# Kernel optimization log

Hardware: AMD Instinct MI355X
Metric: run time of the kernel (lower is better)

Reference implementation:

```python
import jax, jax.numpy as jnp
import numpy as np

B, N, DIM = 4, 2048, 3
H = 128          # hidden
K = 32           # num_neighbours
L = 4            # num_layers
OUT = 6          # out_per_particle


def _dense_init(key, fan_in, fan_out):
    kw, kb = jax.random.split(key)
    w = jax.random.normal(kw, (fan_in, fan_out), jnp.float32) / np.sqrt(fan_in)
    b = jnp.zeros((fan_out,), jnp.float32)
    return w, b


def setup_inputs() -> dict:
    key = jax.random.key(0)
    ks = jax.random.split(key, 8)
    x = jax.random.normal(ks[0], (B, N, DIM), jnp.float32)
    embed_w, embed_b = _dense_init(ks[1], DIM, H)
    # per-layer stacked params
    miw, mib, mow, mob, uiw, uib, uow, uob = [], [], [], [], [], [], [], []
    for l in range(L):
        k0, k1, k2, k3 = jax.random.split(jax.random.fold_in(ks[2], l), 4)
        w, b = _dense_init(k0, 2 * H + 1, H); miw.append(w); mib.append(b)
        w, b = _dense_init(k1, H, H);         mow.append(w); mob.append(b)
        w, b = _dense_init(k2, 2 * H, H);     uiw.append(w); uib.append(b)
        w, b = _dense_init(k3, H, H);         uow.append(w); uob.append(b)
    out_w, out_b = _dense_init(ks[3], H, OUT)
    return {
        'x': x,
        'embed_w': embed_w, 'embed_b': embed_b,
        'msg_in_w': jnp.stack(miw), 'msg_in_b': jnp.stack(mib),
        'msg_out_w': jnp.stack(mow), 'msg_out_b': jnp.stack(mob),
        'upd_in_w': jnp.stack(uiw), 'upd_in_b': jnp.stack(uib),
        'upd_out_w': jnp.stack(uow), 'upd_out_b': jnp.stack(uob),
        'out_w': out_w, 'out_b': out_b,
    }


def reference(x, embed_w, embed_b,
              msg_in_w, msg_in_b, msg_out_w, msg_out_b,
              upd_in_w, upd_in_b, upd_out_w, upd_out_b,
              out_w, out_b):
    act = jax.nn.silu
    n = x.shape[-2]
    # per-particle embed: (B,N,H)
    h = x @ embed_w + embed_b
    # pairwise squared distances (B,N,N), plain Euclidean (geometry=None)
    diff = x[..., :, None, :] - x[..., None, :, :]
    d_sq = jnp.sum(diff * diff, axis=-1)
    eye = jnp.eye(n, dtype=bool)
    d_sq = jnp.where(eye, jnp.inf, d_sq)
    neg_topk, idx_topk = jax.lax.top_k(-d_sq, K)      # (B,N,K)
    d_nearest = jnp.sqrt(jnp.maximum(-neg_topk, 0.0))  # (B,N,K)

    gather = jax.vmap(lambda hb, ib: hb[ib])  # (N,H),(N,K)->(N,K,H) over batch
    n_layers = msg_in_w.shape[0]
    for l in range(n_layers):
        nb = gather(h, idx_topk)                               # (B,N,K,H)
        node_i = jnp.broadcast_to(h[..., :, None, :], nb.shape)
        msg_inp = jnp.concatenate([node_i, nb, d_nearest[..., None]], axis=-1)
        msg = act(msg_inp @ msg_in_w[l] + msg_in_b[l]) @ msg_out_w[l] + msg_out_b[l]
        agg = jnp.sum(msg, axis=-2)                            # (B,N,H)
        upd_inp = jnp.concatenate([h, agg], axis=-1)
        upd = act(upd_inp @ upd_in_w[l] + upd_in_b[l]) @ upd_out_w[l] + upd_out_b[l]
        h = h + upd
    return h @ out_w + out_b
```

## Files before the change

kernel.cpp:

```cpp
#include <hip/hip_runtime.h>
#include <math.h>

#define B_ 4
#define N_ 2048
#define H_ 128
#define K_ 32
#define L_ 4
#define OUT_ 6
#define BN_ (B_*N_)
#define NPB_L 16
#define LBLK 512

typedef __attribute__((ext_vector_type(8))) short short8;
typedef __attribute__((ext_vector_type(4))) float f32x4;

#define LDW (H_ + 8)
#define LAYER_W 98304
#define OFF_W1A 0
#define OFF_W1C 16384
#define OFF_W2  32768
#define OFF_U1  49152
#define OFF_U2  81920
#define SCAP 256
#define KNN_ROWS 4
#define KNN_BLKS (BN_/KNN_ROWS)
#define PREP_BLKS (L_*LAYER_W/256)

#define LOG2E 1.44269504088896340736f
#define LN2   0.69314718055994530942f

__device__ __forceinline__ float silu_f(float x) {
    return __fdividef(x, 1.0f + __expf(-x));
}
__device__ __forceinline__ float silu_y(float y) {
    return __fdividef(y, 1.0f + __builtin_amdgcn_exp2f(-y));
}
__device__ __forceinline__ short f2b(float f) {
    unsigned u = __float_as_uint(f);
    return (short)((u + 0x7FFFu + ((u >> 16) & 1u)) >> 16);
}
__device__ __forceinline__ float b2f(short s) {
    return __uint_as_float(((unsigned)(unsigned short)s) << 16);
}
__device__ __forceinline__ unsigned pack2(short lo, short hi) {
    return (unsigned)(unsigned short)lo | ((unsigned)(unsigned short)hi << 16);
}
__device__ __forceinline__ int mbcnt64(unsigned long long m) {
    return __builtin_amdgcn_mbcnt_hi((unsigned)(m >> 32),
           __builtin_amdgcn_mbcnt_lo((unsigned)m, 0));
}

__global__ __launch_bounds__(256) void k_front(
    const float* __restrict__ x, int* __restrict__ nidx, float* __restrict__ ndist,
    const float* __restrict__ miw, const float* __restrict__ mow,
    const float* __restrict__ uiw, const float* __restrict__ uow,
    short* __restrict__ wt,
    const float* __restrict__ ew, const float* __restrict__ eb,
    const float* __restrict__ mib, float* __restrict__ Epack)
{
    __shared__ float xsx[N_], xsy[N_], xsz[N_];
    __shared__ unsigned skey[KNN_ROWS][SCAP];
    __shared__ int      sid [KNN_ROWS][SCAP];

    if (blockIdx.x >= KNN_BLKS + PREP_BLKS) {
        int t = threadIdx.x;
        int which = t >> 7, n = t & 127;
        const float* W = miw + (size_t)(which ? 128 : 0) * H_;
        float E0 = 0.f, E1 = 0.f, E2 = 0.f, Eb = 0.f;
        for (int k = 0; k < 128; ++k) {
            float w = W[(size_t)k*H_ + n];
            E0 = fmaf(ew[k],       w, E0);
            E1 = fmaf(ew[128 + k], w, E1);
            E2 = fmaf(ew[256 + k], w, E2);
            Eb = fmaf(eb[k],       w, Eb);
        }
        float* dst = Epack + which * 512;
        dst[0*128 + n] = E0 * LOG2E;
        dst[1*128 + n] = E1 * LOG2E;
        dst[2*128 + n] = E2 * LOG2E;
        dst[3*128 + n] = (Eb + (which ? 0.f : mib[n])) * LOG2E;
        return;
    }
    if (blockIdx.x >= KNN_BLKS) {
        int gid = (blockIdx.x - KNN_BLKS) * 256 + threadIdx.x;
        int l = gid / LAYER_W, o = gid - l * LAYER_W;
        float v;
        if (o < OFF_W1C) {
            int n = o >> 7, k = o & 127;
            v = miw[(size_t)l*257*H_ + k*H_ + n] * LOG2E;
        } else if (o < OFF_W2) {
            int oo = o - OFF_W1C, n = oo >> 7, k = oo & 127;
            v = miw[(size_t)l*257*H_ + (128 + k)*H_ + n] * LOG2E;
        } else if (o < OFF_U1) {
            int oo = o - OFF_W2, n = oo >> 7, k = oo & 127;
            v = mow[(size_t)l*H_*H_ + k*H_ + n];
        } else if (o < OFF_U2) {
            int oo = o - OFF_U1, n = oo >> 8, k = oo & 255;
            v = uiw[(size_t)l*2*H_*H_ + k*H_ + n];
        } else {
            int oo = o - OFF_U2, n = oo >> 7, k = oo & 127;
            v = uow[(size_t)l*H_*H_ + k*H_ + n];
        }
        wt[gid] = f2b(v);
        return;
    }

    int b  = blockIdx.x / (N_/KNN_ROWS);
    int i0 = (blockIdx.x % (N_/KNN_ROWS)) * KNN_ROWS;
    const float* xb = x + (size_t)b*N_*3;
    for (int t = threadIdx.x; t < N_*3; t += 256) {
        float v = xb[t];
        int q = t / 3, r = t - q*3;
        float* dst = (r == 0) ? xsx : (r == 1) ? xsy : xsz;
        dst[q] = v;
    }
    __syncthreads();

    int wave = threadIdx.x >> 6, lane = threadIdx.x & 63;
    int i = i0 + wave;
    float xix = xsx[i], xiy = xsy[i], xiz = xsz[i];

    unsigned u[N_/64];
    unsigned lmin = 0xFFFFFFFFu;
#pragma unroll
    for (int t = 0; t < N_/64; ++t) {
        int j = lane + 64*t;
        float d0 = xix-xsx[j], d1 = xiy-xsy[j], d2 = xiz-xsz[j];
        float d = d0*d0 + d1*d1 + d2*d2;
        unsigned k = (j == i) ? 0x7F800000u : __float_as_uint(d);
        u[t] = k;
        lmin = min(lmin, k);
    }
    unsigned mn = lmin, mx = lmin;
    for (int off = 32; off; off >>= 1) {
        unsigned o1 = (unsigned)__shfl_xor((int)mn, off); mn = min(mn, o1);
        unsigned o2 = (unsigned)__shfl_xor((int)mx, off); mx = max(mx, o2);
    }
    unsigned Tup = mn;
    if (mn != mx) {
        int hb = 31 - __clz((int)(mn ^ mx));
        Tup = mn & ~((2u << hb) - 1u);
        for (int bit = hb; bit >= 0; --bit) {
            unsigned cand = Tup | (1u << bit);
            if (__popcll(__ballot(lmin < cand)) < K_) Tup = cand;
        }
    }
    unsigned* sk = skey[wave];
    int*      si = sid [wave];
    int base = 0;
#pragma unroll
    for (int t = 0; t < N_/64; ++t) {
        bool pr = (u[t] <= Tup);
        unsigned long long m = __ballot(pr);
        if (pr) {
            int pos = base + mbcnt64(m);
            if (pos < SCAP) { sk[pos] = u[t]; si[pos] = lane + 64*t; }
        }
        base += __popcll(m);
    }
    int c = min(base, SCAP);
    unsigned sv[4]; int iv[4];
#pragma unroll
    for (int q = 0; q < 4; ++q) {
        int slot = lane + 64*q;
        bool ok = slot < c;
        sv[q] = ok ? sk[slot] : 0xFFFFFFFFu;
        iv[q] = ok ? si[slot] : 0;
    }
    unsigned T = mn;
    if (mn != Tup) {
        int hb = 31 - __clz((int)(mn ^ Tup));
        T = mn & ~((2u << hb) - 1u);
        for (int bit = hb; bit >= 0; --bit) {
            unsigned cand = T | (1u << bit);
            int cnt = __popcll(__ballot(sv[0] < cand)) + __popcll(__ballot(sv[1] < cand))
                    + __popcll(__ballot(sv[2] < cand)) + __popcll(__ballot(sv[3] < cand));
            if (cnt < K_) T = cand;
        }
    }
    int cnt_lt = __popcll(__ballot(sv[0] < T)) + __popcll(__ballot(sv[1] < T))
               + __popcll(__ballot(sv[2] < T)) + __popcll(__ballot(sv[3] < T));
    int need = K_ - cnt_lt;
    size_t rbase = ((size_t)(b*N_ + i)) * K_;
    int ltc = 0, eqc = 0;
#pragma unroll
    for (int q = 0; q < 4; ++q) {
        bool lt = sv[q] < T, eq = sv[q] == T;
        unsigned long long mlt = __ballot(lt), meq = __ballot(eq);
        int pp = ltc + mbcnt64(mlt), ee = eqc + mbcnt64(meq);
        ltc += __popcll(mlt); eqc += __popcll(meq);
        int pos = lt ? pp : ((eq && ee < need) ? (cnt_lt + ee) : -1);
        if (pos >= 0) {
            nidx [rbase + pos] = iv[q];
            ndist[rbase + pos] = sqrtf(__uint_as_float(sv[q]));
        }
    }
}

__global__ __launch_bounds__(LBLK, 4) void k_layer0(
    float* __restrict__ h, short* __restrict__ a,
    const int* __restrict__ nidx, const float* __restrict__ ndist,
    const float* __restrict__ wd,
    const short* __restrict__ wl,
    const float* __restrict__ b2, const float* __restrict__ u1b,
    const float* __restrict__ u2b,
    short* __restrict__ c_wr,
    const short* __restrict__ wn, const float* __restrict__ b1n,
    const float* __restrict__ x, const float* __restrict__ ew,
    const float* __restrict__ eb, const float* __restrict__ Epack)
{
    __shared__ __align__(16) short s_l[NPB_L][LDW];
    __shared__ __align__(16) short h_l[NPB_L][LDW];
    __shared__ __align__(16) short agg_l[NPB_L][LDW];
    __shared__ __align__(16) float h32s[NPB_L][H_];
    __shared__ float xjs[NPB_L][K_][3];
    __shared__ float dst_s[NPB_L][K_];
    int blk = blockIdx.x;
    int batch = (blk & 7) >> 1;
    int sub   = ((blk >> 3) << 1) | (blk & 1);
    int node0 = batch * N_ + sub * NPB_L;
    int tid = threadIdx.x;
    int wave = tid >> 6, lane = tid & 63, l15 = lane & 15, quad = lane >> 4;
    int ncol = wave*16 + l15;

    for (int t = tid; t < NPB_L*H_; t += LBLK) {
        int row = t >> 7, ch = t & 127;
        int gr = node0 + row;
        float v = eb[ch];
        v = fmaf(x[gr*3+0], ew[ch], v);
        v = fmaf(x[gr*3+1], ew[H_+ch], v);
        v = fmaf(x[gr*3+2], ew[2*H_+ch], v);
        h_l[row][ch] = f2b(v);
        h32s[row][ch] = v;
    }
    {
        int j = nidx[(size_t)node0*K_ + tid];
        int sm = tid >> 5, sk = tid & 31;
        dst_s[sm][sk] = ndist[(size_t)node0*K_ + tid];
        const float* xp = x + ((size_t)batch*N_ + j)*3;
        xjs[sm][sk][0] = xp[0]; xjs[sm][sk][1] = xp[1]; xjs[sm][sk][2] = xp[2];
    }
    __syncthreads();

    short8 bw2[4], bu1[8], bu2[4];
#pragma unroll
    for (int kk = 0; kk < 4; ++kk)
        bw2[kk] = *(const short8*)(wl + OFF_W2 + (size_t)ncol*H_ + kk*32 + quad*8);
#pragma unroll
    for (int kk = 0; kk < 8; ++kk)
        bu1[kk] = *(const short8*)(wl + OFF_U1 + (size_t)ncol*2*H_ + kk*32 + quad*8);
#pragma unroll
    for (int kk = 0; kk < 4; ++kk)
        bu2[kk] = *(const short8*)(wl + OFF_U2 + (size_t)ncol*H_ + kk*32 + quad*8);

    {
        float wd0 = wd[2*lane] * LOG2E, wd1 = wd[2*lane+1] * LOG2E;
        int ch0 = 2*lane, ch1 = 2*lane + 1;
        float Ea00 = Epack[ch0],       Ea01 = Epack[ch1];
        float Ea10 = Epack[128+ch0],   Ea11 = Epack[128+ch1];
        float Ea20 = Epack[256+ch0],   Ea21 = Epack[256+ch1];
        float ea0  = Epack[384+ch0],   ea1  = Epack[384+ch1];
        float Ec00 = Epack[512+ch0],   Ec01 = Epack[512+ch1];
        float Ec10 = Epack[640+ch0],   Ec11 = Epack[640+ch1];
        float Ec20 = Epack[768+ch0],   Ec21 = Epack[768+ch1];
        float ec0  = Epack[896+ch0],   ec1  = Epack[896+ch1];
#pragma unroll
        for (int nn = 0; nn < 2; ++nn) {
            int m = wave*2 + nn;
            int gr = node0 + m;
            float xi0 = x[gr*3], xi1 = x[gr*3+1], xi2 = x[gr*3+2];
            float a0 = fmaf(xi2, Ea20, fmaf(xi1, Ea10, fmaf(xi0, Ea00, ea0)));
            float a1 = fmaf(xi2, Ea21, fmaf(xi1, Ea11, fmaf(xi0, Ea01, ea1)));
            float s0 = 0.f, s1 = 0.f;
#pragma unroll
            for (int k = 0; k < K_; ++k) {
                float xj0 = xjs[m][k][0], xj1 = xjs[m][k][1], xj2 = xjs[m][k][2];
                float dd = dst_s[m][k];
                float c0 = fmaf(xj2, Ec20, fmaf(xj1, Ec10, fmaf(xj0, Ec00, ec0)));
                float c1 = fmaf(xj2, Ec21, fmaf(xj1, Ec11, fmaf(xj0, Ec01, ec1)));
                s0 += silu_y(a0 + fmaf(dd, wd0, c0));
                s1 += silu_y(a1 + fmaf(dd, wd1, c1));
            }
            *(unsigned*)&s_l[m][2*lane] = pack2(f2b(s0 * LN2), f2b(s1 * LN2));
        }
    }
    __syncthreads();

    f32x4 acc;
    acc = (f32x4){0,0,0,0};
#pragma unroll
    for (int kk = 0; kk < 4; ++kk) {
        int k0 = kk*32 + quad*8;
        short8 af = *(const short8*)&s_l[l15][k0];
        acc = __builtin_amdgcn_mfma_f32_16x16x32_bf16(af, bw2[kk], acc, 0, 0, 0);
    }
    {
        float b2v = b2[ncol] * (float)K_;
#pragma unroll
        for (int r = 0; r < 4; ++r)
            agg_l[quad*4 + r][ncol] = f2b(acc[r] + b2v);
    }
    __syncthreads();

    acc = (f32x4){0,0,0,0};
#pragma unroll
    for (int kk = 0; kk < 8; ++kk) {
        const short (*src)[LDW] = (kk < 4) ? h_l : agg_l;
        int kloc = ((kk < 4) ? kk*32 : (kk-4)*32) + quad*8;
        short8 af = *(const short8*)&src[l15][kloc];
        acc = __builtin_amdgcn_mfma_f32_16x16x32_bf16(af, bu1[kk], acc, 0, 0, 0);
    }
    short8 bacA[4], bacC[4];
#pragma unroll
    for (int kk = 0; kk < 4; ++kk) {
        bacA[kk] = *(const short8*)(wn + OFF_W1A + (size_t)ncol*H_ + kk*32 + quad*8);
        bacC[kk] = *(const short8*)(wn + OFF_W1C + (size_t)ncol*H_ + kk*32 + quad*8);
    }
    {
        float u1bv = u1b[ncol];
#pragma unroll
        for (int r = 0; r < 4; ++r)
            s_l[quad*4 + r][ncol] = f2b(silu_f(acc[r] + u1bv));
    }
    __syncthreads();

    acc = (f32x4){0,0,0,0};
#pragma unroll
    for (int kk = 0; kk < 4; ++kk) {
        int k0 = kk*32 + quad*8;
        short8 af = *(const short8*)&s_l[l15][k0];
        acc = __builtin_amdgcn_mfma_f32_16x16x32_bf16(af, bu2[kk], acc, 0, 0, 0);
    }
    {
        float u2bv = u2b[ncol];
#pragma unroll
        for (int r = 0; r < 4; ++r) {
            int m = quad*4 + r;
            float nh = h32s[m][ncol] + acc[r] + u2bv;
            h[(size_t)(node0+m)*H_ + ncol] = nh;
            h_l[m][ncol] = f2b(nh);
        }
    }
    __syncthreads();
    {
        int n = ncol;
        f32x4 accA = (f32x4){0,0,0,0}, accC = (f32x4){0,0,0,0};
#pragma unroll
        for (int kk = 0; kk < 4; ++kk) {
            int k0 = kk*32 + quad*8;
            short8 af = *(const short8*)&h_l[l15][k0];
            accA = __builtin_amdgcn_mfma_f32_16x16x32_bf16(af, bacA[kk], accA, 0, 0, 0);
            accC = __builtin_amdgcn_mfma_f32_16x16x32_bf16(af, bacC[kk], accC, 0, 0, 0);
        }
        float b1v = b1n[n] * LOG2E;
#pragma unroll
        for (int r = 0; r < 4; ++r) {
            int m = quad*4 + r;
            size_t gi = (size_t)(node0+m)*H_ + n;
            a[gi]    = f2b(accA[r] + b1v);
            c_wr[gi] = f2b(accC[r]);
        }
    }
}

__global__ __launch_bounds__(LBLK, 4) void k_layer(
    float* __restrict__ h, short* __restrict__ a,
    const int* __restrict__ nidx, const float* __restrict__ ndist,
    const float* __restrict__ wd,
    const short* __restrict__ wl,
    const float* __restrict__ b2, const float* __restrict__ u1b,
    const float* __restrict__ u2b,
    const short* __restrict__ c_rd, short* __restrict__ c_wr,
    const short* __restrict__ wn, const float* __restrict__ b1n, int do_ac,
    const float* __restrict__ ow, const float* __restrict__ ob,
    float* __restrict__ out)
{
    __shared__ __align__(16) short s_l[NPB_L][LDW];
    __shared__ __align__(16) short h_l[NPB_L][LDW];
    __shared__ __align__(16) short agg_l[NPB_L][LDW];
    __shared__ __align__(16) float h32s[NPB_L][H_];
    __shared__ int   idx_s[NPB_L][K_];
    __shared__ float dst_s[NPB_L][K_];
    int blk = blockIdx.x;
    int batch = (blk & 7) >> 1;
    int sub   = ((blk >> 3) << 1) | (blk & 1);
    int node0 = batch * N_ + sub * NPB_L;
    int tid = threadIdx.x;
    int wave = tid >> 6, lane = tid & 63, l15 = lane & 15, quad = lane >> 4;
    int ncol = wave*16 + l15;

    {
        float4 v = reinterpret_cast<const float4*>(h + (size_t)node0*H_)[tid];
        int row = tid >> 5, col = (tid & 31) * 4;
        h_l[row][col+0] = f2b(v.x); h_l[row][col+1] = f2b(v.y);
        h_l[row][col+2] = f2b(v.z); h_l[row][col+3] = f2b(v.w);
        *(float4*)&h32s[row][col] = v;
    }
    idx_s[tid>>5][tid&31] = nidx[(size_t)node0*K_ + tid];
    dst_s[tid>>5][tid&31] = ndist[(size_t)node0*K_ + tid];
    __syncthreads();

    short8 bw2[4], bu1[8], bu2[4];
#pragma unroll
    for (int kk = 0; kk < 4; ++kk)
        bw2[kk] = *(const short8*)(wl + OFF_W2 + (size_t)ncol*H_ + kk*32 + quad*8);
#pragma unroll
    for (int kk = 0; kk < 8; ++kk)
        bu1[kk] = *(const short8*)(wl + OFF_U1 + (size_t)ncol*2*H_ + kk*32 + quad*8);
#pragma unroll
    for (int kk = 0; kk < 4; ++kk)
        bu2[kk] = *(const short8*)(wl + OFF_U2 + (size_t)ncol*H_ + kk*32 + quad*8);

    {
        float wd0 = wd[2*lane] * LOG2E, wd1 = wd[2*lane+1] * LOG2E;
        int wavu = __builtin_amdgcn_readfirstlane(wave);
        const unsigned* c2 = (const unsigned*)c_rd + (size_t)batch*N_*(H_/2);
        const unsigned* a2 = (const unsigned*)a;
#pragma unroll
        for (int nn = 0; nn < 2; ++nn) {
            int m = wavu*2 + nn;
            unsigned av = a2[(size_t)(node0+m)*(H_/2) + lane];
            float a0 = __uint_as_float(av << 16);
            float a1 = __uint_as_float(av & 0xFFFF0000u);
            unsigned cva[16], cvb[16];
#pragma unroll
            for (int k = 0; k < 16; ++k) {
                int j = __builtin_amdgcn_readfirstlane(idx_s[m][k]);
                cva[k] = c2[(size_t)j*(H_/2) + lane];
            }
#pragma unroll
            for (int k = 0; k < 16; ++k) {
                int j = __builtin_amdgcn_readfirstlane(idx_s[m][16+k]);
                cvb[k] = c2[(size_t)j*(H_/2) + lane];
            }
            float s0 = 0.f, s1 = 0.f;
#pragma unroll
            for (int k = 0; k < 16; ++k) {
                float dd = dst_s[m][k];
                s0 += silu_y(a0 + fmaf(dd, wd0, __uint_as_float(cva[k] << 16)));
                s1 += silu_y(a1 + fmaf(dd, wd1, __uint_as_float(cva[k] & 0xFFFF0000u)));
            }
#pragma unroll
            for (int k = 0; k < 16; ++k) {
                float dd = dst_s[m][16+k];
                s0 += silu_y(a0 + fmaf(dd, wd0, __uint_as_float(cvb[k] << 16)));
                s1 += silu_y(a1 + fmaf(dd, wd1, __uint_as_float(cvb[k] & 0xFFFF0000u)));
            }
            *(unsigned*)&s_l[m][2*lane] = pack2(f2b(s0 * LN2), f2b(s1 * LN2));
        }
    }
    __syncthreads();

    f32x4 acc;
    acc = (f32x4){0,0,0,0};
#pragma unroll
    for (int kk = 0; kk < 4; ++kk) {
        int k0 = kk*32 + quad*8;
        short8 af = *(const short8*)&s_l[l15][k0];
        acc = __builtin_amdgcn_mfma_f32_16x16x32_bf16(af, bw2[kk], acc, 0, 0, 0);
    }
    {
        float b2v = b2[ncol] * (float)K_;
#pragma unroll
        for (int r = 0; r < 4; ++r)
            agg_l[quad*4 + r][ncol] = f2b(acc[r] + b2v);
    }
    __syncthreads();

    acc = (f32x4){0,0,0,0};
#pragma unroll
    for (int kk = 0; kk < 8; ++kk) {
        const short (*src)[LDW] = (kk < 4) ? h_l : agg_l;
        int kloc = ((kk < 4) ? kk*32 : (kk-4)*32) + quad*8;
        short8 af = *(const short8*)&src[l15][kloc];
        acc = __builtin_amdgcn_mfma_f32_16x16x32_bf16(af, bu1[kk], acc, 0, 0, 0);
    }
    short8 bacA[4], bacC[4];
    if (do_ac) {
#pragma unroll
        for (int kk = 0; kk < 4; ++kk) {
            bacA[kk] = *(const short8*)(wn + OFF_W1A + (size_t)ncol*H_ + kk*32 + quad*8);
            bacC[kk] = *(const short8*)(wn + OFF_W1C + (size_t)ncol*H_ + kk*32 + quad*8);
        }
    }
    {
        float u1bv = u1b[ncol];
#pragma unroll
        for (int r = 0; r < 4; ++r)
            s_l[quad*4 + r][ncol] = f2b(silu_f(acc[r] + u1bv));
    }
    __syncthreads();

    acc = (f32x4){0,0,0,0};
#pragma unroll
    for (int kk = 0; kk < 4; ++kk) {
        int k0 = kk*32 + quad*8;
        short8 af = *(const short8*)&s_l[l15][k0];
        acc = __builtin_amdgcn_mfma_f32_16x16x32_bf16(af, bu2[kk], acc, 0, 0, 0);
    }
    {
        float u2bv = u2b[ncol];
#pragma unroll
        for (int r = 0; r < 4; ++r) {
            int m = quad*4 + r;
            float nh = h32s[m][ncol] + acc[r] + u2bv;
            h[(size_t)(node0+m)*H_ + ncol] = nh;
            if (do_ac) h_l[m][ncol] = f2b(nh);
            else       h32s[m][ncol] = nh;
        }
    }
    if (do_ac) {
        __syncthreads();
        int n = ncol;
        f32x4 accA = (f32x4){0,0,0,0}, accC = (f32x4){0,0,0,0};
#pragma unroll
        for (int kk = 0; kk < 4; ++kk) {
            int k0 = kk*32 + quad*8;
            short8 af = *(const short8*)&h_l[l15][k0];
            accA = __builtin_amdgcn_mfma_f32_16x16x32_bf16(af, bacA[kk], accA, 0, 0, 0);
            accC = __builtin_amdgcn_mfma_f32_16x16x32_bf16(af, bacC[kk], accC, 0, 0, 0);
        }
        float b1v = b1n[n] * LOG2E;
#pragma unroll
        for (int r = 0; r < 4; ++r) {
            int m = quad*4 + r;
            size_t gi = (size_t)(node0+m)*H_ + n;
            a[gi]    = f2b(accA[r] + b1v);
            c_wr[gi] = f2b(accC[r]);
        }
    } else {
        __syncthreads();
        int node = tid >> 5, s = tid & 31;
        float p0=0.f,p1=0.f,p2=0.f,p3=0.f,p4=0.f,p5=0.f;
#pragma unroll
        for (int q = 0; q < 4; ++q) {
            int r = s + q*32;
            float hv = h32s[node][r];
            const float* owr = ow + r*OUT_;
            p0 = fmaf(hv, owr[0], p0); p1 = fmaf(hv, owr[1], p1);
            p2 = fmaf(hv, owr[2], p2); p3 = fmaf(hv, owr[3], p3);
            p4 = fmaf(hv, owr[4], p4); p5 = fmaf(hv, owr[5], p5);
        }
#pragma unroll
        for (int off = 16; off; off >>= 1) {
            p0 += __shfl_xor(p0, off); p1 += __shfl_xor(p1, off);
            p2 += __shfl_xor(p2, off); p3 += __shfl_xor(p3, off);
            p4 += __shfl_xor(p4, off); p5 += __shfl_xor(p5, off);
        }
        if (s == 0) {
            float* op = out + (size_t)(node0+node)*OUT_;
            op[0] = p0 + ob[0]; op[1] = p1 + ob[1]; op[2] = p2 + ob[2];
            op[3] = p3 + ob[3]; op[4] = p4 + ob[4]; op[5] = p5 + ob[5];
        }
    }
}

extern "C" void kernel_launch(void* const* d_in, const int* in_sizes, int n_in,
                              void* d_out, int out_size, void* d_ws, size_t ws_size,
                              hipStream_t stream)
{
    const float* x   = (const float*)d_in[0];
    const float* ew  = (const float*)d_in[1];
    const float* eb  = (const float*)d_in[2];
    const float* miw = (const float*)d_in[3];
    const float* mib = (const float*)d_in[4];
    const float* mow = (const float*)d_in[5];
    const float* mob = (const float*)d_in[6];
    const float* uiw = (const float*)d_in[7];
    const float* uib = (const float*)d_in[8];
    const float* uow = (const float*)d_in[9];
    const float* uob = (const float*)d_in[10];
    const float* ow  = (const float*)d_in[11];
    const float* ob  = (const float*)d_in[12];
    float* out = (float*)d_out;

    char* w = (char*)d_ws;
    float* h  = (float*)w;                         w += (size_t)BN_*H_*4;
    float* nd = (float*)w;                         w += (size_t)BN_*K_*4;
    int*   ni = (int*)w;                           w += (size_t)BN_*K_*4;
    short* a  = (short*)w;                         w += (size_t)BN_*H_*2;
    short* c0 = (short*)w;                         w += (size_t)BN_*H_*2;
    short* c1 = (short*)w;                         w += (size_t)BN_*H_*2;
    short* wt = (short*)w;                         w += (size_t)L_*LAYER_W*2;
    float* Epack = (float*)w;

    k_front<<<KNN_BLKS + PREP_BLKS + 1, 256, 0, stream>>>(x, ni, nd,
        miw, mow, uiw, uow, wt, ew, eb, mib, Epack);
    k_layer0<<<BN_/NPB_L, LBLK, 0, stream>>>(h, a, ni, nd,
        miw + 256*H_, wt,
        mob, uib, uob,
        c1, wt + LAYER_W, mib + H_,
        x, ew, eb, Epack);
    for (int l = 1; l < L_; ++l) {
        const short* c_rd = (l & 1) ? c1 : c0;
        short*       c_wr = (l & 1) ? c0 : c1;
        int do_ac = (l + 1 < L_);
        const short* wn = wt + (size_t)(do_ac ? (l+1) : l) * LAYER_W;
        const float* b1n = mib + (size_t)(do_ac ? (l+1) : l) * H_;
        k_layer<<<BN_/NPB_L, LBLK, 0, stream>>>(h, a, ni, nd,
            miw + (size_t)l*257*H_ + 256*H_,
            wt + (size_t)l*LAYER_W,
            mob + (size_t)l*H_, uib + (size_t)l*H_, uob + (size_t)l*H_,
            c_rd, c_wr, wn, b1n, do_ac,
            ow, ob, out);
    }
}
```

Measured before the change: 218.9 us.

## Replace specialized layer0 kernel with tiny prep kernel and deepen neighbour gather prefetch

Removes the dedicated layer-0 kernel that recomputed the neighbour projections from raw coordinates. A small elementwise kernel now writes h, a and c for layer 0, so all four layers run through the generic gather-based layer kernel. Inside that kernel, all 64 neighbour rows for both nodes of a wave are loaded before any SiLU accumulation, and the update weight loads move after the message phase. This gives more memory-level parallelism per wave and shortens live ranges during the gather, at the cost of an extra launch and a gather pass in layer 0 in place of the cheap coordinate-based recompute. It also raises register pressure from the 64-entry buffer.

```diff
diff --git a/kernel.cpp b/kernel.cpp
--- a/kernel.cpp
+++ b/kernel.cpp
@@ -197,170 +197,31 @@
     }
 }
 
-__global__ __launch_bounds__(LBLK, 4) void k_layer0(
-    float* __restrict__ h, short* __restrict__ a,
-    const int* __restrict__ nidx, const float* __restrict__ ndist,
-    const float* __restrict__ wd,
-    const short* __restrict__ wl,
-    const float* __restrict__ b2, const float* __restrict__ u1b,
-    const float* __restrict__ u2b,
-    short* __restrict__ c_wr,
-    const short* __restrict__ wn, const float* __restrict__ b1n,
+__global__ __launch_bounds__(512) void k_prep0(
+    float* __restrict__ h, short* __restrict__ a, short* __restrict__ c0,
     const float* __restrict__ x, const float* __restrict__ ew,
     const float* __restrict__ eb, const float* __restrict__ Epack)
 {
-    __shared__ __align__(16) short s_l[NPB_L][LDW];
-    __shared__ __align__(16) short h_l[NPB_L][LDW];
-    __shared__ __align__(16) short agg_l[NPB_L][LDW];
-    __shared__ __align__(16) float h32s[NPB_L][H_];
-    __shared__ float xjs[NPB_L][K_][3];
-    __shared__ float dst_s[NPB_L][K_];
-    int blk = blockIdx.x;
-    int batch = (blk & 7) >> 1;
-    int sub   = ((blk >> 3) << 1) | (blk & 1);
-    int node0 = batch * N_ + sub * NPB_L;
-    int tid = threadIdx.x;
-    int wave = tid >> 6, lane = tid & 63, l15 = lane & 15, quad = lane >> 4;
-    int ncol = wave*16 + l15;
-
-    for (int t = tid; t < NPB_L*H_; t += LBLK) {
-        int row = t >> 7, ch = t & 127;
-        int gr = node0 + row;
-        float v = eb[ch];
-        v = fmaf(x[gr*3+0], ew[ch], v);
-        v = fmaf(x[gr*3+1], ew[H_+ch], v);
-        v = fmaf(x[gr*3+2], ew[2*H_+ch], v);
-        h_l[row][ch] = f2b(v);
-        h32s[row][ch] = v;
-    }
-    {
-        int j = nidx[(size_t)node0*K_ + tid];
-        int sm = tid >> 5, sk = tid & 31;
-        dst_s[sm][sk] = ndist[(size_t)node0*K_ + tid];
-        const float* xp = x + ((size_t)batch*N_ + j)*3;
-        xjs[sm][sk][0] = xp[0]; xjs[sm][sk][1] = xp[1]; xjs[sm][sk][2] = xp[2];
-    }
-    __syncthreads();
-
-    short8 bw2[4], bu1[8], bu2[4];
-#pragma unroll
-    for (int kk = 0; kk < 4; ++kk)
-        bw2[kk] = *(const short8*)(wl + OFF_W2 + (size_t)ncol*H_ + kk*32 + quad*8);
-#pragma unroll
-    for (int kk = 0; kk < 8; ++kk)
-        bu1[kk] = *(const short8*)(wl + OFF_U1 + (size_t)ncol*2*H_ + kk*32 + quad*8);
-#pragma unroll
-    for (int kk = 0; kk < 4; ++kk)
-        bu2[kk] = *(const short8*)(wl + OFF_U2 + (size_t)ncol*H_ + kk*32 + quad*8);
-
-    {
-        float wd0 = wd[2*lane] * LOG2E, wd1 = wd[2*lane+1] * LOG2E;
-        int ch0 = 2*lane, ch1 = 2*lane + 1;
-        float Ea00 = Epack[ch0],       Ea01 = Epack[ch1];
-        float Ea10 = Epack[128+ch0],   Ea11 = Epack[128+ch1];
-        float Ea20 = Epack[256+ch0],   Ea21 = Epack[256+ch1];
-        float ea0  = Epack[384+ch0],   ea1  = Epack[384+ch1];
-        float Ec00 = Epack[512+ch0],   Ec01 = Epack[512+ch1];
-        float Ec10 = Epack[640+ch0],   Ec11 = Epack[640+ch1];
-        float Ec20 = Epack[768+ch0],   Ec21 = Epack[768+ch1];
-        float ec0  = Epack[896+ch0],   ec1  = Epack[896+ch1];
-#pragma unroll
-        for (int nn = 0; nn < 2; ++nn) {
-            int m = wave*2 + nn;
-            int gr = node0 + m;
-            float xi0 = x[gr*3], xi1 = x[gr*3+1], xi2 = x[gr*3+2];
-            float a0 = fmaf(xi2, Ea20, fmaf(xi1, Ea10, fmaf(xi0, Ea00, ea0)));
-            float a1 = fmaf(xi2, Ea21, fmaf(xi1, Ea11, fmaf(xi0, Ea01, ea1)));
-            float s0 = 0.f, s1 = 0.f;
-#pragma unroll
-            for (int k = 0; k < K_; ++k) {
-                float xj0 = xjs[m][k][0], xj1 = xjs[m][k][1], xj2 = xjs[m][k][2];
-                float dd = dst_s[m][k];
-                float c0 = fmaf(xj2, Ec20, fmaf(xj1, Ec10, fmaf(xj0, Ec00, ec0)));
-                float c1 = fmaf(xj2, Ec21, fmaf(xj1, Ec11, fmaf(xj0, Ec01, ec1)));
-                s0 += silu_y(a0 + fmaf(dd, wd0, c0));
-                s1 += silu_y(a1 + fmaf(dd, wd1, c1));
-            }
-            *(unsigned*)&s_l[m][2*lane] = pack2(f2b(s0 * LN2), f2b(s1 * LN2));
-        }
-    }
-    __syncthreads();
-
-    f32x4 acc;
-    acc = (f32x4){0,0,0,0};
-#pragma unroll
-    for (int kk = 0; kk < 4; ++kk) {
-        int k0 = kk*32 + quad*8;
-        short8 af = *(const short8*)&s_l[l15][k0];
-        acc = __builtin_amdgcn_mfma_f32_16x16x32_bf16(af, bw2[kk], acc, 0, 0, 0);
-    }
-    {
-        float b2v = b2[ncol] * (float)K_;
-#pragma unroll
-        for (int r = 0; r < 4; ++r)
-            agg_l[quad*4 + r][ncol] = f2b(acc[r] + b2v);
-    }
-    __syncthreads();
-
-    acc = (f32x4){0,0,0,0};
-#pragma unroll
-    for (int kk = 0; kk < 8; ++kk) {
-        const short (*src)[LDW] = (kk < 4) ? h_l : agg_l;
-        int kloc = ((kk < 4) ? kk*32 : (kk-4)*32) + quad*8;
-        short8 af = *(const short8*)&src[l15][kloc];
-        acc = __builtin_amdgcn_mfma_f32_16x16x32_bf16(af, bu1[kk], acc, 0, 0, 0);
-    }
-    short8 bacA[4], bacC[4];
-#pragma unroll
-    for (int kk = 0; kk < 4; ++kk) {
-        bacA[kk] = *(const short8*)(wn + OFF_W1A + (size_t)ncol*H_ + kk*32 + quad*8);
-        bacC[kk] = *(const short8*)(wn + OFF_W1C + (size_t)ncol*H_ + kk*32 + quad*8);
-    }
-    {
-        float u1bv = u1b[ncol];
-#pragma unroll
-        for (int r = 0; r < 4; ++r)
-            s_l[quad*4 + r][ncol] = f2b(silu_f(acc[r] + u1bv));
-    }
-    __syncthreads();
-
-    acc = (f32x4){0,0,0,0};
-#pragma unroll
-    for (int kk = 0; kk < 4; ++kk) {
-        int k0 = kk*32 + quad*8;
-        short8 af = *(const short8*)&s_l[l15][k0];
-        acc = __builtin_amdgcn_mfma_f32_16x16x32_bf16(af, bu2[kk], acc, 0, 0, 0);
-    }
-    {
-        float u2bv = u2b[ncol];
-#pragma unroll
-        for (int r = 0; r < 4; ++r) {
-            int m = quad*4 + r;
-            float nh = h32s[m][ncol] + acc[r] + u2bv;
-            h[(size_t)(node0+m)*H_ + ncol] = nh;
-            h_l[m][ncol] = f2b(nh);
-        }
-    }
-    __syncthreads();
-    {
-        int n = ncol;
-        f32x4 accA = (f32x4){0,0,0,0}, accC = (f32x4){0,0,0,0};
-#pragma unroll
-        for (int kk = 0; kk < 4; ++kk) {
-            int k0 = kk*32 + quad*8;
-            short8 af = *(const short8*)&h_l[l15][k0];
-            accA = __builtin_amdgcn_mfma_f32_16x16x32_bf16(af, bacA[kk], accA, 0, 0, 0);
-            accC = __builtin_amdgcn_mfma_f32_16x16x32_bf16(af, bacC[kk], accC, 0, 0, 0);
-        }
-        float b1v = b1n[n] * LOG2E;
-#pragma unroll
-        for (int r = 0; r < 4; ++r) {
-            int m = quad*4 + r;
-            size_t gi = (size_t)(node0+m)*H_ + n;
-            a[gi]    = f2b(accA[r] + b1v);
-            c_wr[gi] = f2b(accC[r]);
-        }
-    }
+    int t = blockIdx.x * 512 + threadIdx.x;
+    int node = t >> 7, ch = t & 127;
+    const float* xp = x + (size_t)node*3;
+    float x0 = xp[0], x1 = xp[1], x2 = xp[2];
+    float hv = eb[ch];
+    hv = fmaf(x0, ew[ch],       hv);
+    hv = fmaf(x1, ew[H_+ch],    hv);
+    hv = fmaf(x2, ew[2*H_+ch],  hv);
+    float av = Epack[384+ch];
+    av = fmaf(x0, Epack[ch],     av);
+    av = fmaf(x1, Epack[128+ch], av);
+    av = fmaf(x2, Epack[256+ch], av);
+    float cv = Epack[896+ch];
+    cv = fmaf(x0, Epack[512+ch], cv);
+    cv = fmaf(x1, Epack[640+ch], cv);
+    cv = fmaf(x2, Epack[768+ch], cv);
+    size_t gi = (size_t)node*H_ + ch;
+    h[gi]  = hv;
+    a[gi]  = f2b(av);
+    c0[gi] = f2b(cv);
 }
 
 __global__ __launch_bounds__(LBLK, 4) void k_layer(
@@ -400,55 +261,62 @@
     dst_s[tid>>5][tid&31] = ndist[(size_t)node0*K_ + tid];
     __syncthreads();
 
-    short8 bw2[4], bu1[8], bu2[4];
+    short8 bw2[4];
 #pragma unroll
     for (int kk = 0; kk < 4; ++kk)
         bw2[kk] = *(const short8*)(wl + OFF_W2 + (size_t)ncol*H_ + kk*32 + quad*8);
-#pragma unroll
-    for (int kk = 0; kk < 8; ++kk)
-        bu1[kk] = *(const short8*)(wl + OFF_U1 + (size_t)ncol*2*H_ + kk*32 + quad*8);
-#pragma unroll
-    for (int kk = 0; kk < 4; ++kk)
-        bu2[kk] = *(const short8*)(wl + OFF_U2 + (size_t)ncol*H_ + kk*32 + quad*8);
 
     {
         float wd0 = wd[2*lane] * LOG2E, wd1 = wd[2*lane+1] * LOG2E;
         int wavu = __builtin_amdgcn_readfirstlane(wave);
         const unsigned* c2 = (const unsigned*)c_rd + (size_t)batch*N_*(H_/2);
         const unsigned* a2 = (const unsigned*)a;
-#pragma unroll
-        for (int nn = 0; nn < 2; ++nn) {
-            int m = wavu*2 + nn;
-            unsigned av = a2[(size_t)(node0+m)*(H_/2) + lane];
-            float a0 = __uint_as_float(av << 16);
-            float a1 = __uint_as_float(av & 0xFFFF0000u);
-            unsigned cva[16], cvb[16];
-#pragma unroll
-            for (int k = 0; k < 16; ++k) {
-                int j = __builtin_amdgcn_readfirstlane(idx_s[m][k]);
-                cva[k] = c2[(size_t)j*(H_/2) + lane];
+        int m0 = wavu*2, m1 = wavu*2 + 1;
+        unsigned av0 = a2[(size_t)(node0+m0)*(H_/2) + lane];
+        unsigned av1 = a2[(size_t)(node0+m1)*(H_/2) + lane];
+        unsigned cv0[K_], cv1[K_];
+#pragma unroll
+        for (int k = 0; k < K_; ++k) {
+            int j = __builtin_amdgcn_readfirstlane(idx_s[m0][k]);
+            cv0[k] = c2[(size_t)j*(H_/2) + lane];
+        }
+#pragma unroll
+        for (int k = 0; k < K_; ++k) {
+            int j = __builtin_amdgcn_readfirstlane(idx_s[m1][k]);
+            cv1[k] = c2[(size_t)j*(H_/2) + lane];
+        }
+        {
+            float a0 = __uint_as_float(av0 << 16);
+            float a1 = __uint_as_float(av0 & 0xFFFF0000u);
+            float s0 = 0.f, s1 = 0.f;
+#pragma unroll
+            for (int k = 0; k < K_; ++k) {
+                float dd = dst_s[m0][k];
+                s0 += silu_y(a0 + fmaf(dd, wd0, __uint_as_float(cv0[k] << 16)));
+                s1 += silu_y(a1 + fmaf(dd, wd1, __uint_as_float(cv0[k] & 0xFFFF0000u)));
             }
-#pragma unroll
-            for (int k = 0; k < 16; ++k) {
-                int j = __builtin_amdgcn_readfirstlane(idx_s[m][16+k]);
-                cvb[k] = c2[(size_t)j*(H_/2) + lane];
+            *(unsigned*)&s_l[m0][2*lane] = pack2(f2b(s0 * LN2), f2b(s1 * LN2));
+        }
+        {
+            float a0 = __uint_as_float(av1 << 16);
+            float a1 = __uint_as_float(av1 & 0xFFFF0000u);
+            float s0 = 0.f, s1 = 0.f;
+#pragma unroll
+            for (int k = 0; k < K_; ++k) {
+                float dd = dst_s[m1][k];
+                s0 += silu_y(a0 + fmaf(dd, wd0, __uint_as_float(cv1[k] << 16)));
+                s1 += silu_y(a1 + fmaf(dd, wd1, __uint_as_float(cv1[k] & 0xFFFF0000u)));
             }
-            float s0 = 0.f, s1 = 0.f;
-#pragma unroll
-            for (int k = 0; k < 16; ++k) {
-                float dd = dst_s[m][k];
-                s0 += silu_y(a0 + fmaf(dd, wd0, __uint_as_float(cva[k] << 16)));
-                s1 += silu_y(a1 + fmaf(dd, wd1, __uint_as_float(cva[k] & 0xFFFF0000u)));
-            }
-#pragma unroll
-            for (int k = 0; k < 16; ++k) {
-                float dd = dst_s[m][16+k];
-                s0 += silu_y(a0 + fmaf(dd, wd0, __uint_as_float(cvb[k] << 16)));
-                s1 += silu_y(a1 + fmaf(dd, wd1, __uint_as_float(cvb[k] & 0xFFFF0000u)));
-            }
-            *(unsigned*)&s_l[m][2*lane] = pack2(f2b(s0 * LN2), f2b(s1 * LN2));
-        }
-    }
+            *(unsigned*)&s_l[m1][2*lane] = pack2(f2b(s0 * LN2), f2b(s1 * LN2));
+        }
+    }
+    short8 bu1[8], bu2[4];
+#pragma unroll
+    for (int kk = 0; kk < 8; ++kk)
+        bu1[kk] = *(const short8*)(wl + OFF_U1 + (size_t)ncol*2*H_ + kk*32 + quad*8);
+#pragma unroll
+    for (int kk = 0; kk < 4; ++kk)
+        bu2[kk] = *(const short8*)(wl + OFF_U2 + (size_t)ncol*H_ + kk*32 + quad*8);
     __syncthreads();
 
     f32x4 acc;
@@ -586,12 +454,8 @@
 
     k_front<<<KNN_BLKS + PREP_BLKS + 1, 256, 0, stream>>>(x, ni, nd,
         miw, mow, uiw, uow, wt, ew, eb, mib, Epack);
-    k_layer0<<<BN_/NPB_L, LBLK, 0, stream>>>(h, a, ni, nd,
-        miw + 256*H_, wt,
-        mob, uib, uob,
-        c1, wt + LAYER_W, mib + H_,
-        x, ew, eb, Epack);
-    for (int l = 1; l < L_; ++l) {
+    k_prep0<<<BN_*H_/512, 512, 0, stream>>>(h, a, c0, x, ew, eb, Epack);
+    for (int l = 0; l < L_; ++l) {
         const short* c_rd = (l & 1) ? c1 : c0;
         short*       c_wr = (l & 1) ? c0 : c1;
         int do_ac = (l + 1 < L_);
```

New measurement: 224.8 us. 1.03x slower.
